# Kernel tuning notes

Hardware: AMD Instinct MI355X
Metric: run time of the kernel (lower is better)

## Reference

```python
import jax, jax.numpy as jnp
import numpy as np

CAUSAL = True


def setup_inputs() -> dict:
    key = jax.random.key(0)
    k1, k2, k3 = jax.random.split(key, 3)
    B, S, D_IN, D_INNER, D_OUT = 4, 4096, 512, 64, 512
    x = jax.random.normal(k1, (B, S, D_IN), dtype=jnp.float32)
    W_qkv = jax.random.normal(k2, (D_IN, 3 * D_INNER), dtype=jnp.float32) * (D_IN ** -0.5)
    W_out = jax.random.normal(k3, (D_INNER, D_OUT), dtype=jnp.float32) * (D_INNER ** -0.5)
    b_out = jnp.zeros((D_OUT,), dtype=jnp.float32)
    return {"x": x, "W_qkv": W_qkv, "W_out": W_out, "b_out": b_out}


def reference(x, W_qkv, W_out, b_out):
    d_inner = W_out.shape[0]
    scale = d_inner ** -0.5
    qkv = jnp.einsum('bsi,io->bso', x, W_qkv)  # [B,S,3*d_inner]
    q, k, v = jnp.split(qkv, 3, axis=-1)
    sim = jnp.einsum('bid,bjd->bij', q, k) * scale  # [B,S,S]
    if CAUSAL:
        S = x.shape[1]
        mask = jnp.triu(jnp.ones((S, S), dtype=bool), k=1)
        sim = jnp.where(mask[None], -jnp.finfo(q.dtype).max, sim)
    attn = jax.nn.softmax(sim, axis=-1)
    out = jnp.einsum('bij,bjd->bid', attn, v)  # [B,S,d_inner]
    return jnp.einsum('bid,do->bio', out, W_out) + b_out
```

## Files before the change

kernel.cpp:

```cpp
#include <hip/hip_runtime.h>
#include <math.h>

typedef __attribute__((ext_vector_type(8))) short short8;
typedef __attribute__((ext_vector_type(4))) short short4v;
typedef __attribute__((ext_vector_type(4))) float f32x4;
typedef __attribute__((ext_vector_type(4))) float float4v;
typedef __attribute__((ext_vector_type(2))) unsigned int uint2v;

__device__ __forceinline__ unsigned short f2bf(float f){
  unsigned int u = __float_as_uint(f);
  u += 0x7FFFu + ((u >> 16) & 1u);
  return (unsigned short)(u >> 16);
}
__device__ __forceinline__ float bf2f(short s){
  return __uint_as_float(((unsigned int)(unsigned short)s) << 16);
}
__device__ __forceinline__ unsigned int cvtpk(float lo, float hi){
  unsigned int r;
  asm("v_cvt_pk_bf16_f32 %0, %1, %2" : "=v"(r) : "v"(lo), "v"(hi));
  return r;
}

typedef __attribute__((address_space(1))) const unsigned char* gas_t;
typedef __attribute__((address_space(3))) unsigned char* las_t;
__device__ __forceinline__ void async16(const void* g, void* l) {
  __builtin_amdgcn_global_load_lds((gas_t)g, (las_t)l, 16, 0, 0);
}

#define SC2 0.1803368801111204f

__global__ __launch_bounds__(256) void prep_w(
    const float* __restrict__ Wqkv, const float* __restrict__ Wout,
    unsigned short* __restrict__ Wtq, unsigned short* __restrict__ Wto)
{
  int idx = blockIdx.x * 256 + threadIdx.x;
  if (idx < 192 * 512) {
    int n = idx >> 9, k = idx & 511;
    Wtq[idx] = f2bf(Wqkv[k * 192 + n]);
  } else {
    int i2 = idx - 192 * 512;
    int n = i2 >> 6, k = i2 & 63;
    Wto[i2] = f2bf(Wout[k * 512 + n]);
  }
}

__global__ __launch_bounds__(256) void qkv_kernel(
    const float* __restrict__ x,
    const unsigned short* __restrict__ Wt,
    unsigned short* __restrict__ qg,
    unsigned short* __restrict__ kg,
    unsigned short* __restrict__ vT)
{
  __shared__ __align__(16) unsigned short Wb[2][64][128];
  __shared__ __align__(16) unsigned short vbuf[64][72];
  const int part = blockIdx.x % 3;
  const int rb   = blockIdx.x / 3;
  const int lane = threadIdx.x & 63;
  const int wave = threadIdx.x >> 6;
  const int mrow = lane & 15;
  const int quad = lane >> 4;
  const int mb = rb * 64;
  const int m0 = mb + wave * 16;
  const int sw = mrow & 7;

  const int srow = lane >> 4;
  const int sch  = lane & 15;
#define STAGE_W(s, dst)                                                       \
  {                                                                           \
    _Pragma("unroll")                                                         \
    for (int ii = 0; ii < 4; ii++) {                                          \
      const int r0 = wave * 16 + ii * 4;                                      \
      const int r  = r0 + srow;                                               \
      const int cd = (sch & 8) | ((sch ^ (r & 7)) & 7);                       \
      async16(Wt + (size_t)(part * 64 + r) * 512 + (s) * 128 + cd * 8,        \
              (dst) + r0 * 128);                                              \
    }                                                                         \
  }

  STAGE_W(0, &Wb[0][0][0])

  f32x4 acc[4];
#pragma unroll
  for (int t = 0; t < 4; t++) acc[t] = (f32x4){0.f, 0.f, 0.f, 0.f};
  const float* xp = x + (size_t)(m0 + mrow) * 512 + quad * 8;

  for (int s = 0; s < 4; s++) {
    __syncthreads();
    if (s < 3) STAGE_W(s + 1, &Wb[(s + 1) & 1][0][0])
    const unsigned short* Wc = &Wb[s & 1][0][0];
#pragma unroll
    for (int l = 0; l < 4; l++) {
      const int kk = s * 4 + l;
      float4v a0 = *(const float4v*)(xp + kk * 32);
      float4v a1 = *(const float4v*)(xp + kk * 32 + 4);
      short8 af;
#pragma unroll
      for (int j = 0; j < 4; j++) { af[j] = (short)f2bf(a0[j]); af[4 + j] = (short)f2bf(a1[j]); }
      const int c   = l * 4 + quad;
      const int pos = (c & 8) | ((c ^ sw) & 7);
#pragma unroll
      for (int t = 0; t < 4; t++) {
        short8 bf = *(const short8*)(Wc + (t * 16 + mrow) * 128 + pos * 8);
        acc[t] = __builtin_amdgcn_mfma_f32_16x16x32_bf16(af, bf, acc[t], 0, 0, 0);
      }
    }
  }

  const float osc = (part == 0) ? SC2 : 1.0f;
  __syncthreads();
#pragma unroll
  for (int t = 0; t < 4; t++)
#pragma unroll
    for (int r = 0; r < 4; r++)
      vbuf[wave * 16 + quad * 4 + r][t * 16 + mrow] = f2bf(acc[t][r] * osc);
  __syncthreads();

  if (part < 2) {
    unsigned short* dst = part ? kg : qg;
    const int row = threadIdx.x >> 2;
    const int seg = (threadIdx.x & 3) * 16;
    short8 w0 = *(const short8*)&vbuf[row][seg];
    short8 w1 = *(const short8*)&vbuf[row][seg + 8];
    unsigned short* p = dst + (size_t)(mb + row) * 64 + seg;
    *(short8*)(p) = w0;
    *(short8*)(p + 8) = w1;
  } else {
    const int d  = threadIdx.x >> 2;
    const int s8 = (threadIdx.x & 3) * 16;
    const int bb = rb >> 6;
    const int sb = mb & 4095;
    short8 w0, w1;
#pragma unroll
    for (int i = 0; i < 8; i++) {
      w0[i] = (short)vbuf[s8 + i][d];
      w1[i] = (short)vbuf[s8 + 8 + i][d];
    }
    unsigned short* dst = vT + (size_t)bb * (64 * 4096) + (size_t)d * 4096 + sb + s8;
    *(short8*)(dst) = w0;
    *(short8*)(dst + 8) = w1;
  }
#undef STAGE_W
}

template <bool MASKED>
__device__ __forceinline__ void soft_pv(
    const f32x4* sA, const short8* vf, int kb, int qlane, int quad, int mrow,
    float& lacc, f32x4* o, unsigned short (*pb)[72])
{
  float p[16];
#pragma unroll
  for (int t = 0; t < 4; t++)
#pragma unroll
    for (int r = 0; r < 4; r++) {
      float v = sA[t][r];
      if (MASKED && (kb + t * 16 + quad * 4 + r > qlane)) v = -3.0e38f;
      p[t * 4 + r] = exp2f(v);
    }
  float ps = 0.f;
#pragma unroll
  for (int i = 0; i < 16; i++) ps += p[i];
  lacc += ps;
#pragma unroll
  for (int t = 0; t < 4; t++) {
    unsigned int d0 = cvtpk(p[t * 4 + 0], p[t * 4 + 1]);
    unsigned int d1 = cvtpk(p[t * 4 + 2], p[t * 4 + 3]);
    *(uint2v*)&pb[mrow][t * 16 + quad * 4] = (uint2v){d0, d1};
  }
  short8 pf0 = *(const short8*)&pb[mrow][quad * 8];
  short8 pf1 = *(const short8*)&pb[mrow][32 + quad * 8];
#pragma unroll
  for (int c = 0; c < 4; c++) {
    o[c] = __builtin_amdgcn_mfma_f32_16x16x32_bf16(vf[2 * c],     pf0, o[c], 0, 0, 0);
    o[c] = __builtin_amdgcn_mfma_f32_16x16x32_bf16(vf[2 * c + 1], pf1, o[c], 0, 0, 0);
  }
}

__global__ __launch_bounds__(512) void attn_kernel(
    const unsigned short* __restrict__ qg,
    const unsigned short* __restrict__ kg,
    const unsigned short* __restrict__ vT,
    unsigned short* __restrict__ Opart,
    float* __restrict__ lpart)
{
  __shared__ __align__(16) unsigned short Kb[2][64][64];
  __shared__ __align__(16) unsigned short Vb[2][64][64];
  __shared__ __align__(16) unsigned short pbuf[8][16][72];
  const int lane = threadIdx.x & 63;
  const int wave = threadIdx.x >> 6;
  const int mrow = lane & 15;
  const int quad = lane >> 4;
  const int sw   = mrow & 7;

  int t = 143 - (blockIdx.x % 144);
  const int b = blockIdx.x / 144;
  int qj = 31, c = 0;
  for (int qq = 0; qq < 32; qq++) {
    const int ncq = (qq >> 2) + 1;
    if (t < ncq) { qj = qq; c = t; break; }
    t -= ncq;
  }

  const int sq0w = qj * 128 + wave * 16;
  const int g0w  = b * 4096 + sq0w;

  short8 qf[2];
  {
    const unsigned short* qp = qg + (size_t)(g0w + mrow) * 64 + quad * 8;
    qf[0] = *(const short8*)(qp);
    qf[1] = *(const short8*)(qp + 32);
  }

  const int kstart = c << 9;
  const int qend   = qj * 128 + 128;
  const int kend   = (kstart + 512 < qend) ? (kstart + 512) : qend;
  const int nTb    = (kend - kstart) >> 6;

  f32x4 o[4];
#pragma unroll
  for (int ct = 0; ct < 4; ct++) o[ct] = (f32x4){0.f, 0.f, 0.f, 0.f};
  float lr = 0.f;

  const unsigned short* kbase = kg + (size_t)b * 4096 * 64;
  const unsigned short* vbase = vT + (size_t)b * 64 * 4096;
  const int shalf = lane >> 3;
  const int sch   = lane & 7;

#define STAGE_KV(kb, Kd, Vd)                                                  \
  {                                                                           \
    const int r0 = wave * 8;                                                  \
    const int r  = r0 + shalf;                                                \
    const int cd = sch ^ (r & 7);                                             \
    async16(kbase + (size_t)((kb) + r) * 64 + cd * 8, (Kd) + r0 * 64);        \
    async16(vbase + (size_t)r * 4096 + (kb) + cd * 8, (Vd) + r0 * 64);        \
  }

  STAGE_KV(kstart, &Kb[0][0][0], &Vb[0][0][0])
  __syncthreads();

  for (int j = 0; j < nTb; j++) {
    const int kb = kstart + 64 * j;
    if (j + 1 < nTb)
      STAGE_KV(kb + 64, &Kb[(j + 1) & 1][0][0], &Vb[(j + 1) & 1][0][0])
    const unsigned short* Kc = &Kb[j & 1][0][0];
    const unsigned short* Vc = &Vb[j & 1][0][0];

    const bool act = (kb <= sq0w + 15);
    if (act) {
      short8 kf[8];
#pragma unroll
      for (int tt = 0; tt < 4; tt++) {
        const unsigned short* kr = Kc + (tt * 16 + mrow) * 64;
        kf[2 * tt]     = *(const short8*)(kr + (quad ^ sw) * 8);
        kf[2 * tt + 1] = *(const short8*)(kr + ((quad + 4) ^ sw) * 8);
      }
      f32x4 sA[4];
#pragma unroll
      for (int tt = 0; tt < 4; tt++) {
        f32x4 z = (f32x4){0.f, 0.f, 0.f, 0.f};
        z = __builtin_amdgcn_mfma_f32_16x16x32_bf16(kf[2 * tt],     qf[0], z, 0, 0, 0);
        z = __builtin_amdgcn_mfma_f32_16x16x32_bf16(kf[2 * tt + 1], qf[1], z, 0, 0, 0);
        sA[tt] = z;
      }
      short8 vf[8];
#pragma unroll
      for (int cc = 0; cc < 4; cc++) {
        const unsigned short* vr = Vc + (cc * 16 + mrow) * 64;
        vf[2 * cc]     = *(const short8*)(vr + (quad ^ sw) * 8);
        vf[2 * cc + 1] = *(const short8*)(vr + ((quad + 4) ^ sw) * 8);
      }
      if (kb + 63 <= sq0w)
        soft_pv<false>(sA, vf, kb, sq0w + mrow, quad, mrow, lr, o, pbuf[wave]);
      else
        soft_pv<true> (sA, vf, kb, sq0w + mrow, quad, mrow, lr, o, pbuf[wave]);
    }
    __syncthreads();
  }
#undef STAGE_KV

  {
    float lt = lr;
    lt += __shfl_xor(lt, 16);
    lt += __shfl_xor(lt, 32);
    const size_t row = (size_t)c * 16384 + g0w + mrow;
#pragma unroll
    for (int ct = 0; ct < 4; ct++) {
      short4v ob;
#pragma unroll
      for (int r = 0; r < 4; r++) ob[r] = (short)f2bf(o[ct][r]);
      *(short4v*)(Opart + row * 64 + ct * 16 + quad * 4) = ob;
    }
    if (quad == 0) lpart[row] = lt;
  }
}

__global__ __launch_bounds__(256) void combine_kernel(
    const unsigned short* __restrict__ Opart,
    const float* __restrict__ lpart,
    const unsigned short* __restrict__ WtO,
    const float* __restrict__ bias,
    float* __restrict__ out)
{
  __shared__ __align__(16) unsigned short Wob[256][64];
  __shared__ __align__(16) float obuf[4][16][132];
  const int lane = threadIdx.x & 63;
  const int wave = threadIdx.x >> 6;
  const int mrow = lane & 15;
  const int quad = lane >> 4;
  const int rb   = blockIdx.x >> 1;
  const int half = blockIdx.x & 1;
  const int g0 = rb * 64 + wave * 16;
  const int nc = ((g0 & 4095) >> 9) + 1;

  {
    const int hl  = lane >> 3;
    const int chp = lane & 7;
#pragma unroll
    for (int ii = 0; ii < 8; ii++) {
      const int r0 = wave * 64 + ii * 8;
      const int r  = r0 + hl;
      const int cd = chp ^ (r & 7);
      async16(WtO + (size_t)(half * 256 + r) * 64 + cd * 8, &Wob[r0][0]);
    }
  }

  float L = 0.f;
  f32x4 A0 = (f32x4){0,0,0,0}, A1 = A0, A2 = A0, A3 = A0;
  for (int cI = 0; cI < nc; cI++) {
    const size_t row = (size_t)cI * 16384 + g0 + mrow;
    L += lpart[row];
    const unsigned short* op = Opart + row * 64 + quad * 8;
    short8 x0 = *(const short8*)(op);
    short8 x1 = *(const short8*)(op + 32);
#pragma unroll
    for (int j = 0; j < 4; j++) {
      A0[j] += bf2f(x0[j]); A1[j] += bf2f(x0[4 + j]);
      A2[j] += bf2f(x1[j]); A3[j] += bf2f(x1[4 + j]);
    }
  }
  const float inv = 1.0f / L;
  short8 of0, of1;
#pragma unroll
  for (int i = 0; i < 4; i++) {
    of0[i]     = (short)f2bf(A0[i] * inv);
    of0[i + 4] = (short)f2bf(A1[i] * inv);
    of1[i]     = (short)f2bf(A2[i] * inv);
    of1[i + 4] = (short)f2bf(A3[i] * inv);
  }
  __syncthreads();

  const int sw = mrow & 7;
  for (int chi = 0; chi < 2; chi++) {
    const int ch = half * 2 + chi;
#pragma unroll
    for (int t = 0; t < 8; t++) {
      const int n = ch * 128 + t * 16 + mrow;
      const unsigned short* wr = &Wob[chi * 128 + t * 16 + mrow][0];
      short8 w0 = *(const short8*)(wr + (quad ^ sw) * 8);
      short8 w1 = *(const short8*)(wr + ((quad + 4) ^ sw) * 8);
      f32x4 pr = (f32x4){0,0,0,0};
      pr = __builtin_amdgcn_mfma_f32_16x16x32_bf16(of0, w0, pr, 0, 0, 0);
      pr = __builtin_amdgcn_mfma_f32_16x16x32_bf16(of1, w1, pr, 0, 0, 0);
      const float bv = bias[n];
#pragma unroll
      for (int r = 0; r < 4; r++)
        obuf[wave][quad * 4 + r][t * 16 + mrow] = pr[r] + bv;
    }
#pragma unroll
    for (int j = 0; j < 4; j++) {
#pragma unroll
      for (int h = 0; h < 2; h++) {
        const int row = 4 * j + (lane >> 4);
        const int col = 4 * (lane & 15) + 64 * h;
        float4v v = *(const float4v*)&obuf[wave][row][col];
        *(float4v*)(out + (size_t)(g0 + row) * 512 + ch * 128 + col) = v;
      }
    }
  }
}

extern "C" void kernel_launch(void* const* d_in, const int* in_sizes, int n_in,
                              void* d_out, int out_size, void* d_ws, size_t ws_size,
                              hipStream_t stream) {
  const float* x    = (const float*)d_in[0];
  const float* Wqkv = (const float*)d_in[1];
  const float* Wout = (const float*)d_in[2];
  const float* bout = (const float*)d_in[3];
  float* out = (float*)d_out;

  unsigned short* q   = (unsigned short*)d_ws;
  unsigned short* k   = q   + 16384 * 64;
  unsigned short* vT  = k   + 16384 * 64;
  unsigned short* Wtq = vT  + 4 * 64 * 4096;
  unsigned short* Wto = Wtq + 192 * 512;
  unsigned short* Opart = Wto + 512 * 64;
  float* lprt = (float*)(Opart + (size_t)8 * 16384 * 64);

  prep_w<<<512, 256, 0, stream>>>(Wqkv, Wout, Wtq, Wto);
  qkv_kernel<<<768, 256, 0, stream>>>(x, Wtq, q, k, vT);
  attn_kernel<<<576, 512, 0, stream>>>(q, k, vT, Opart, lprt);
  combine_kernel<<<512, 256, 0, stream>>>(Opart, lprt, Wto, bout, out);
}
```

Baseline: 135.5 us.

## Process two 16-row query strips per wave to reuse staged K/V tiles

Each wave now handles 32 query rows (two 16-row strips) instead of 16, so a block covers 256 query rows and the grid halves to 288 blocks. K and V fragments loaded from shared memory are reused across both strips, which halves the global K/V staging traffic and the shared-memory fragment reads per query row. In exchange, register pressure goes up from the doubled accumulators and Q fragments. With only 288 blocks on a large GPU, occupancy and load balance also get worse, and the causal tail work is coarser.

After: 147.0 us. 8.5% more time.

```diff
diff --git a/kernel.cpp b/kernel.cpp
--- a/kernel.cpp
+++ b/kernel.cpp
@@ -191,34 +191,37 @@
   const int quad = lane >> 4;
   const int sw   = mrow & 7;
 
-  int t = 143 - (blockIdx.x % 144);
-  const int b = blockIdx.x / 144;
-  int qj = 31, c = 0;
-  for (int qq = 0; qq < 32; qq++) {
-    const int ncq = (qq >> 2) + 1;
-    if (t < ncq) { qj = qq; c = t; break; }
+  int t = 71 - (blockIdx.x % 72);
+  const int b = blockIdx.x / 72;
+  int qb = 15, c = 0;
+  for (int qq = 0; qq < 16; qq++) {
+    const int ncq = (qq >> 1) + 1;
+    if (t < ncq) { qb = qq; c = t; break; }
     t -= ncq;
   }
 
-  const int sq0w = qj * 128 + wave * 16;
+  const int sq0w = qb * 256 + wave * 32;
   const int g0w  = b * 4096 + sq0w;
 
-  short8 qf[2];
-  {
-    const unsigned short* qp = qg + (size_t)(g0w + mrow) * 64 + quad * 8;
-    qf[0] = *(const short8*)(qp);
-    qf[1] = *(const short8*)(qp + 32);
+  short8 qf[2][2];
+#pragma unroll
+  for (int s = 0; s < 2; s++) {
+    const unsigned short* qp = qg + (size_t)(g0w + 16 * s + mrow) * 64 + quad * 8;
+    qf[s][0] = *(const short8*)(qp);
+    qf[s][1] = *(const short8*)(qp + 32);
   }
 
   const int kstart = c << 9;
-  const int qend   = qj * 128 + 128;
+  const int qend   = qb * 256 + 256;
   const int kend   = (kstart + 512 < qend) ? (kstart + 512) : qend;
   const int nTb    = (kend - kstart) >> 6;
 
-  f32x4 o[4];
-#pragma unroll
-  for (int ct = 0; ct < 4; ct++) o[ct] = (f32x4){0.f, 0.f, 0.f, 0.f};
-  float lr = 0.f;
+  f32x4 o[2][4];
+#pragma unroll
+  for (int s = 0; s < 2; s++)
+#pragma unroll
+    for (int ct = 0; ct < 4; ct++) o[s][ct] = (f32x4){0.f, 0.f, 0.f, 0.f};
+  float lr[2] = {0.f, 0.f};
 
   const unsigned short* kbase = kg + (size_t)b * 4096 * 64;
   const unsigned short* vbase = vT + (size_t)b * 64 * 4096;
@@ -244,8 +247,8 @@
     const unsigned short* Kc = &Kb[j & 1][0][0];
     const unsigned short* Vc = &Vb[j & 1][0][0];
 
-    const bool act = (kb <= sq0w + 15);
-    if (act) {
+    const bool anyact = (kb <= sq0w + 32 - 1);
+    if (anyact) {
       short8 kf[8];
 #pragma unroll
       for (int tt = 0; tt < 4; tt++) {
@@ -253,13 +256,20 @@
         kf[2 * tt]     = *(const short8*)(kr + (quad ^ sw) * 8);
         kf[2 * tt + 1] = *(const short8*)(kr + ((quad + 4) ^ sw) * 8);
       }
-      f32x4 sA[4];
-#pragma unroll
-      for (int tt = 0; tt < 4; tt++) {
-        f32x4 z = (f32x4){0.f, 0.f, 0.f, 0.f};
-        z = __builtin_amdgcn_mfma_f32_16x16x32_bf16(kf[2 * tt],     qf[0], z, 0, 0, 0);
-        z = __builtin_amdgcn_mfma_f32_16x16x32_bf16(kf[2 * tt + 1], qf[1], z, 0, 0, 0);
-        sA[tt] = z;
+      f32x4 sA[2][4];
+      bool act[2];
+#pragma unroll
+      for (int s = 0; s < 2; s++) {
+        act[s] = (kb <= sq0w + 16 * s + 15);
+        if (act[s]) {
+#pragma unroll
+          for (int tt = 0; tt < 4; tt++) {
+            f32x4 z = (f32x4){0.f, 0.f, 0.f, 0.f};
+            z = __builtin_amdgcn_mfma_f32_16x16x32_bf16(kf[2 * tt],     qf[s][0], z, 0, 0, 0);
+            z = __builtin_amdgcn_mfma_f32_16x16x32_bf16(kf[2 * tt + 1], qf[s][1], z, 0, 0, 0);
+            sA[s][tt] = z;
+          }
+        }
       }
       short8 vf[8];
 #pragma unroll
@@ -268,25 +278,31 @@
         vf[2 * cc]     = *(const short8*)(vr + (quad ^ sw) * 8);
         vf[2 * cc + 1] = *(const short8*)(vr + ((quad + 4) ^ sw) * 8);
       }
-      if (kb + 63 <= sq0w)
-        soft_pv<false>(sA, vf, kb, sq0w + mrow, quad, mrow, lr, o, pbuf[wave]);
-      else
-        soft_pv<true> (sA, vf, kb, sq0w + mrow, quad, mrow, lr, o, pbuf[wave]);
+#pragma unroll
+      for (int s = 0; s < 2; s++) {
+        if (!act[s]) continue;
+        const int qlo = sq0w + 16 * s;
+        if (kb + 63 <= qlo)
+          soft_pv<false>(sA[s], vf, kb, qlo + mrow, quad, mrow, lr[s], o[s], pbuf[wave]);
+        else
+          soft_pv<true> (sA[s], vf, kb, qlo + mrow, quad, mrow, lr[s], o[s], pbuf[wave]);
+      }
     }
     __syncthreads();
   }
 #undef STAGE_KV
 
-  {
-    float lt = lr;
+#pragma unroll
+  for (int s = 0; s < 2; s++) {
+    float lt = lr[s];
     lt += __shfl_xor(lt, 16);
     lt += __shfl_xor(lt, 32);
-    const size_t row = (size_t)c * 16384 + g0w + mrow;
+    const size_t row = (size_t)c * 16384 + g0w + 16 * s + mrow;
 #pragma unroll
     for (int ct = 0; ct < 4; ct++) {
       short4v ob;
 #pragma unroll
-      for (int r = 0; r < 4; r++) ob[r] = (short)f2bf(o[ct][r]);
+      for (int r = 0; r < 4; r++) ob[r] = (short)f2bf(o[s][ct][r]);
       *(short4v*)(Opart + row * 64 + ct * 16 + quad * 4) = ob;
     }
     if (quad == 0) lpart[row] = lt;
@@ -397,6 +413,6 @@
 
   prep_w<<<512, 256, 0, stream>>>(Wqkv, Wout, Wtq, Wto);
   qkv_kernel<<<768, 256, 0, stream>>>(x, Wtq, q, k, vT);
-  attn_kernel<<<576, 512, 0, stream>>>(q, k, vT, Opart, lprt);
+  attn_kernel<<<288, 512, 0, stream>>>(q, k, vT, Opart, lprt);
   combine_kernel<<<512, 256, 0, stream>>>(Opart, lprt, Wto, bout, out);
 }
```
